# Kernel optimization log

Measured on AMD Instinct MI355X. Metric: run time of the kernel, lower is better.

Reference implementation:

```python
import jax, jax.numpy as jnp
from jax import lax
import numpy as np

T = 8
TAU = 2.0       # LIFNode tau
VTH = 1.0       # v_threshold for IF and LIF
ALPHA = 2.0     # surrogate.ATan default alpha
BN_EPS = 1e-5

# --- ATan surrogate-gradient heaviside (spikingjelly semantics) ---
@jax.custom_vjp
def heaviside_atan(x):
    return (x >= 0.0).astype(x.dtype)

def _h_fwd(x):
    return heaviside_atan(x), x

def _h_bwd(x, g):
    sg = (ALPHA / 2.0) / (1.0 + (jnp.pi / 2.0 * ALPHA * x) ** 2)
    return (g * sg,)

heaviside_atan.defvjp(_h_fwd, _h_bwd)

# --- multi-step IF node: v += x; spike; hard reset to 0 ---
def if_node(x_seq):
    def step(v, x):
        v = v + x
        s = heaviside_atan(v - VTH)
        return (1.0 - s) * v, s
    return lax.scan(step, jnp.zeros_like(x_seq[0]), x_seq)[1]

# --- multi-step LIF node (decay_input=True, v_reset=0, hard reset) ---
def lif_node(x_seq):
    def step(v, x):
        v = v + (x - v) / TAU
        s = heaviside_atan(v - VTH)
        return (1.0 - s) * v, s
    return lax.scan(step, jnp.zeros_like(x_seq[0]), x_seq)[1]

def conv2d(x, w, b):
    y = lax.conv_general_dilated(x, w, (1, 1), 'SAME', dimension_numbers=('NCHW', 'OIHW', 'NCHW'))
    return y + b[None, :, None, None]

def bn(x, g, b, m, v):
    scale = g * lax.rsqrt(v + BN_EPS)
    return (x - m[None, :, None, None]) * scale[None, :, None, None] + b[None, :, None, None]

def maxpool2(x):
    return lax.reduce_window(x, -jnp.inf, lax.max, (1, 1, 2, 2), (1, 1, 2, 2), 'VALID')


def setup_inputs():
    key = jax.random.key(0)
    ks = jax.random.split(key, 8)
    B = 32
    f32 = jnp.float32
    d = {}
    d['x'] = jax.random.normal(ks[0], (B, 1, 48, 48), f32)
    d['conv1_w'] = jax.random.normal(ks[1], (128, 1, 3, 3), f32) * 0.2
    d['conv1_b'] = jnp.zeros((128,), f32)
    d['bn1_g'] = jnp.ones((128,), f32)
    d['bn1_b'] = jnp.zeros((128,), f32)
    d['bn1_m'] = jnp.zeros((128,), f32)
    d['bn1_v'] = jnp.ones((128,), f32)
    d['conv2_w'] = jax.random.normal(ks[2], (128, 128, 3, 3), f32) * 0.03
    d['conv2_b'] = jnp.zeros((128,), f32)
    d['bn2_g'] = jnp.ones((128,), f32)
    d['bn2_b'] = jnp.zeros((128,), f32)
    d['bn2_m'] = jnp.zeros((128,), f32)
    d['bn2_v'] = jnp.ones((128,), f32)
    d['fc1_w'] = jax.random.normal(ks[3], (1152, 128 * 12 * 12), f32) * 0.007
    d['fc1_b'] = jnp.zeros((1152,), f32)
    d['fc2_w'] = jax.random.normal(ks[4], (128, 1152), f32) * 0.03
    d['fc2_b'] = jnp.zeros((128,), f32)
    d['fc3_w'] = jax.random.normal(ks[5], (7, 128), f32) * 0.09
    d['fc3_b'] = jnp.zeros((7,), f32)
    return d


def reference(x, conv1_w, conv1_b, bn1_g, bn1_b, bn1_m, bn1_v,
              conv2_w, conv2_b, bn2_g, bn2_b, bn2_m, bn2_v,
              fc1_w, fc1_b, fc2_w, fc2_b, fc3_w, fc3_b):
    B = x.shape[0]
    # layer1 (single-step): conv + BN (eval-mode), dropout is identity at eval
    h = bn(conv2d(x, conv1_w, conv1_b), bn1_g, bn1_b, bn1_m, bn1_v)  # [B,128,48,48]
    # repeat over T timesteps
    x_step = jnp.broadcast_to(h, (T,) + h.shape)                      # [T,B,128,48,48]
    # layer2: IF -> maxpool -> conv -> BN -> IF -> maxpool
    s1 = if_node(x_step)                                              # [T,B,128,48,48]
    p1 = maxpool2(s1.reshape((T * B,) + s1.shape[2:]))                # [T*B,128,24,24]
    c2 = bn(conv2d(p1, conv2_w, conv2_b), bn2_g, bn2_b, bn2_m, bn2_v)
    s2 = if_node(c2.reshape((T, B) + c2.shape[1:]))                   # [T,B,128,24,24]
    p2 = maxpool2(s2.reshape((T * B,) + s2.shape[2:]))                # [T*B,128,12,12]
    # layer3: flatten -> fc -> LIF -> fc -> LIF -> fc -> LIF
    f = p2.reshape(T, B, -1)                                          # [T,B,18432]
    l1 = lif_node(jnp.einsum('tbi,oi->tbo', f, fc1_w) + fc1_b)        # [T,B,1152]
    l2 = lif_node(jnp.einsum('tbi,oi->tbo', l1, fc2_w) + fc2_b)       # [T,B,128]
    l3 = lif_node(jnp.einsum('tbi,oi->tbo', l2, fc3_w) + fc3_b)       # [T,B,7]
    return l3.mean(axis=0)                                            # [B,7]
```

## Files before the change

### kernel.cpp

```cpp
#include <hip/hip_runtime.h>
#include <hip/hip_bf16.h>


typedef float  f32x4  __attribute__((ext_vector_type(4)));
typedef __bf16 bf16x8 __attribute__((ext_vector_type(8)));

#define T_STEPS 8

static const size_t OFF_P1    = 0;
static const size_t OFF_PART  = 0;
static const size_t OFF_WT    = 44302336;
static const size_t OFF_P2    = 45481984;
static const size_t OFF_W2T   = 54919168;
static const size_t OFF_L1S   = 55508992;

__device__ __forceinline__ unsigned short bf16_rne(float f) {
  unsigned u = __builtin_bit_cast(unsigned, f);
  u += 0x7FFFu + ((u >> 16) & 1u);
  return (unsigned short)(u >> 16);
}
__device__ __forceinline__ float bf16_to_f(unsigned short h) {
  unsigned u = ((unsigned)h) << 16;
  return __builtin_bit_cast(float, u);
}

__device__ __forceinline__ void split_pair(float f0, float f1, unsigned& hi, unsigned& lo) {
  __hip_bfloat162 h2 = __float22bfloat162_rn(make_float2(f0, f1));
  unsigned uh; __builtin_memcpy(&uh, &h2, 4);
  float g0 = __builtin_bit_cast(float, uh << 16);
  float g1 = __builtin_bit_cast(float, uh & 0xFFFF0000u);
  __hip_bfloat162 l2 = __float22bfloat162_rn(make_float2(f0 - g0, f1 - g1));
  unsigned ul; __builtin_memcpy(&ul, &l2, 4);
  hi = uh;
  lo = ul;
}

__device__ __forceinline__ void lds_load16(const void* g, void* l) {
  auto* gp = reinterpret_cast<const __attribute__((address_space(1))) unsigned int*>(
      reinterpret_cast<uintptr_t>(g));
  auto* lp = reinterpret_cast<__attribute__((address_space(3))) unsigned int*>(
      reinterpret_cast<uintptr_t>(l));
  __builtin_amdgcn_global_load_lds(gp, lp, 16, 0, 0);
}

__global__ __launch_bounds__(256) void prep_conv1(
    const float* __restrict__ conv2_w, const float* __restrict__ fc2_w,
    short* __restrict__ wt_hi, short* __restrict__ wt_lo, float* __restrict__ w2t,
    uint4* __restrict__ p1pad4,
    const float* __restrict__ x, const float* __restrict__ w1, const float* __restrict__ b1,
    const float* __restrict__ g1, const float* __restrict__ be1, const float* __restrict__ m1,
    const float* __restrict__ vv1, short* __restrict__ p1) {
  __shared__ float patch[2][16];
  const int bx = blockIdx.x;
  if (bx < 2752) {
    int i = bx * 256 + threadIdx.x;
    if (i < 147456) {
      int tap = i >> 14;
      int oc  = (i >> 7) & 127;
      int ic  = i & 127;
      float wv = conv2_w[oc * 1152 + ic * 9 + tap];
      unsigned short h = bf16_rne(wv);
      wt_hi[i] = (short)h;
      wt_lo[i] = (short)bf16_rne(wv - bf16_to_f(h));
    } else if (i < 294912) {
      int j = i - 147456;
      int o = j & 127, k = j >> 7;
      w2t[j] = fc2_w[o * 1152 + k];
    } else {
      int k = i - 294912;
      int tb = k / 1600;
      int rem = k - tb * 1600;
      int pos = rem >> 4, c8 = rem & 15;
      int y, xx;
      if (pos < 26)      { y = 0;  xx = pos; }
      else if (pos < 52) { y = 25; xx = pos - 26; }
      else { int jj = pos - 52; y = 1 + (jj >> 1); xx = (jj & 1) * 25; }
      p1pad4[(tb * 676 + y * 26 + xx) * 16 + c8] = make_uint4(0u, 0u, 0u, 0u);
    }
    return;
  }
  const int bid  = bx - 2752;
  const int b    = bid / 288;
  const int spp  = bid - b * 288;
  const int half = threadIdx.x >> 7;
  const int sp   = spp * 2 + half;
  const int c    = threadIdx.x & 127;
  const int oy = sp / 24, ox = sp % 24;
  if (c < 16) {
    int py = c >> 2, px = c & 3;
    int iy = 2 * oy - 1 + py, ix = 2 * ox - 1 + px;
    float v = 0.f;
    if (iy >= 0 && iy < 48 && ix >= 0 && ix < 48) v = x[b * 2304 + iy * 48 + ix];
    patch[half][c] = v;
  }
  __syncthreads();
  float w[9];
#pragma unroll
  for (int i = 0; i < 9; ++i) w[i] = w1[c * 9 + i];
  float scale = g1[c] * rsqrtf(vv1[c] + 1e-5f);
  float shift = (b1[c] - m1[c]) * scale + be1[c];
  float h[4];
#pragma unroll
  for (int p = 0; p < 4; ++p) {
    int py = p >> 1, px = p & 1;
    float s = 0.f;
#pragma unroll
    for (int dy = 0; dy < 3; ++dy)
#pragma unroll
      for (int dx = 0; dx < 3; ++dx) s += patch[half][(py + dy) * 4 + (px + dx)] * w[dy * 3 + dx];
    h[p] = s * scale + shift;
  }
  float va = 0.f, vb = 0.f, vc = 0.f, vd = 0.f;
  size_t base = ((size_t)b * 676 + (size_t)(1 + oy) * 26 + (1 + ox)) * 128 + c;
#pragma unroll
  for (int t = 0; t < T_STEPS; ++t) {
    va += h[0]; vb += h[1]; vc += h[2]; vd += h[3];
    bool s0 = va >= 1.f, s1 = vb >= 1.f, s2 = vc >= 1.f, s3 = vd >= 1.f;
    p1[base + (size_t)t * (32 * 676 * 128)] = (s0 | s1 | s2 | s3) ? (short)0x3F80 : (short)0;
    if (s0) va = 0.f; if (s1) vb = 0.f; if (s2) vc = 0.f; if (s3) vd = 0.f;
  }
}

__global__ __launch_bounds__(256, 2) void conv2_gemm(
    const short* __restrict__ p1pad, const short* __restrict__ wt_hi, const short* __restrict__ wt_lo,
    const float* __restrict__ conv2_b, const float* __restrict__ bn2_g, const float* __restrict__ bn2_b,
    const float* __restrict__ bn2_m, const float* __restrict__ bn2_v, short* __restrict__ p2) {
  __shared__ __align__(16) short lds[32768];
  short* ldsA  = lds;
  short* ldsBh = lds + 16384;
  short* ldsBl = lds + 24576;

  const int tid = threadIdx.x;
  const int lane = tid & 63;
  const int w = tid >> 6;
  const int wm = w & 1, wn = w >> 1;
  const int b  = blockIdx.x;
  const int sp = blockIdx.y;
  const int gy = sp / 3;
  const int gx = sp - gy * 3;

  const int g = (lane & 7) ^ (lane >> 3);
  int rowofsA[8], bofs[4];
#pragma unroll
  for (int j = 0; j < 8; ++j) {
    int r = w * 64 + j * 8 + (lane >> 3);
    int t = r >> 5, iy = (r >> 3) & 3, ix = r & 7;
    rowofsA[j] = (((t * 32 + b) * 676) + (4 * gy + iy) * 26 + (8 * gx + ix)) * 128 + g * 8;
  }
#pragma unroll
  for (int j = 0; j < 4; ++j) {
    int n = w * 32 + j * 8 + (lane >> 3);
    bofs[j] = n * 128 + g * 8;
  }

  f32x4 acc[8][4];
#pragma unroll
  for (int mi = 0; mi < 8; ++mi)
#pragma unroll
    for (int ni = 0; ni < 4; ++ni) acc[mi][ni] = (f32x4){0.f, 0.f, 0.f, 0.f};

#pragma unroll 1
  for (int s = 0; s < 18; ++s) {
    const int tap = s >> 1;
    const int kk = (s & 1) << 6;
    const int tapoff = ((tap / 3) * 26 + (tap % 3)) * 128;
    __syncthreads();
#pragma unroll
    for (int j = 0; j < 8; ++j) {
      lds_load16(p1pad + rowofsA[j] + tapoff + kk, ldsA + (w * 64 + j * 8) * 64 + lane * 8);
    }
    const int wtoff = tap * 16384 + kk;
#pragma unroll
    for (int j = 0; j < 4; ++j) {
      lds_load16(wt_hi + wtoff + bofs[j], ldsBh + (w * 32 + j * 8) * 64 + lane * 8);
      lds_load16(wt_lo + wtoff + bofs[j], ldsBl + (w * 32 + j * 8) * 64 + lane * 8);
    }
    __syncthreads();
#pragma unroll
    for (int ks = 0; ks < 2; ++ks) {
      const int cch = ks * 4 + (lane >> 4);
      bf16x8 a[8], bh[4], bl[4];
#pragma unroll
      for (int i = 0; i < 8; ++i) {
        int r = wm * 128 + i * 16 + (lane & 15);
        a[i] = *(const bf16x8*)(ldsA + r * 64 + ((cch ^ (r & 7)) * 8));
      }
#pragma unroll
      for (int i = 0; i < 4; ++i) {
        int n = wn * 64 + i * 16 + (lane & 15);
        bh[i] = *(const bf16x8*)(ldsBh + n * 64 + ((cch ^ (n & 7)) * 8));
        bl[i] = *(const bf16x8*)(ldsBl + n * 64 + ((cch ^ (n & 7)) * 8));
      }
#pragma unroll
      for (int mi = 0; mi < 8; ++mi)
#pragma unroll
        for (int ni = 0; ni < 4; ++ni) {
          acc[mi][ni] = __builtin_amdgcn_mfma_f32_16x16x32_bf16(a[mi], bh[ni], acc[mi][ni], 0, 0, 0);
          acc[mi][ni] = __builtin_amdgcn_mfma_f32_16x16x32_bf16(a[mi], bl[ni], acc[mi][ni], 0, 0, 0);
        }
    }
  }

  float sc[4], sh[4];
#pragma unroll
  for (int ni = 0; ni < 4; ++ni) {
    int oc = wn * 64 + ni * 16 + (lane & 15);
    sc[ni] = bn2_g[oc] * rsqrtf(bn2_v[oc] + 1e-5f);
    sh[ni] = (conv2_b[oc] - bn2_m[oc]) * sc[ni] + bn2_b[oc];
  }
  float* ybuf = (float*)lds;
  const int S = 132;
  float v[32];
#pragma unroll
  for (int q = 0; q < 32; ++q) v[q] = 0.f;
  unsigned short* p2u = (unsigned short*)p2;
  __syncthreads();
#pragma unroll
  for (int q = 0; q < 4; ++q) {
    if (wm == (q >> 1)) {
      const int mib = (q & 1) * 4;
#pragma unroll
      for (int ml = 0; ml < 4; ++ml)
#pragma unroll
        for (int ni = 0; ni < 4; ++ni)
#pragma unroll
          for (int r = 0; r < 4; ++r) {
            int lam = ml * 16 + ((lane >> 4) << 2) + r;
            int col = wn * 64 + ni * 16 + (lane & 15);
            ybuf[lam * S + col] = acc[mib + ml][ni][r] * sc[ni] + sh[ni];
          }
    }
    __syncthreads();
    if (tid < 128) {
      const int oc = tid;
#pragma unroll
      for (int tt = 0; tt < 2; ++tt) {
        int t = 2 * q + tt;
#pragma unroll
        for (int pooly = 0; pooly < 2; ++pooly) {
          unsigned short ov[4];
#pragma unroll
          for (int poolx = 0; poolx < 4; ++poolx) {
            bool any = false;
#pragma unroll
            for (int ry = 0; ry < 2; ++ry)
#pragma unroll
              for (int rx = 0; rx < 2; ++rx) {
                int iy = 2 * pooly + ry, ix = 2 * poolx + rx;
                float xx = ybuf[(tt * 32 + iy * 8 + ix) * S + oc];
                int qi = iy * 8 + ix;
                v[qi] += xx;
                bool ss = v[qi] >= 1.f;
                any |= ss;
                if (ss) v[qi] = 0.f;
              }
            ov[poolx] = any ? (unsigned short)0x3F80 : (unsigned short)0;
          }
          ushort4 o4; o4.x = ov[0]; o4.y = ov[1]; o4.z = ov[2]; o4.w = ov[3];
          *(ushort4*)(p2u + ((size_t)(t * 32 + b) * 128 + oc) * 144 + (2 * gy + pooly) * 12 + 4 * gx) = o4;
        }
      }
    }
    __syncthreads();
  }
}

__global__ __launch_bounds__(512) void fc1_gemm(const short* __restrict__ p2,
                                                const float* __restrict__ fc1_w,
                                                float* __restrict__ part) {
  __shared__ __align__(16) short lds[24576];
  short* ldsA = lds;
  short* ldsBh = lds + 16384;
  short* ldsBl = lds + 20480;

  const int tid = threadIdx.x;
  const int lane = tid & 63;
  const int w = tid >> 6;
  const int wm = w & 3, wn = w >> 2;
  const int nt2 = blockIdx.x;
  const int n0 = nt2 * 64;
  const int kb = blockIdx.y * 576;

  const int g = (lane & 7) ^ (lane >> 3);
  int aofs[4];
#pragma unroll
  for (int j = 0; j < 4; ++j) {
    int r = w * 32 + j * 8 + (lane >> 3);
    aofs[j] = r * 18432 + g * 8;
  }
  const int bn = tid >> 3;
  const int c0 = tid & 7;
  const float* wrow = fc1_w + (size_t)(n0 + bn) * 18432 + c0 * 8;
  const int bpos = (c0 ^ (bn & 7)) * 8;

  f32x4 acc[4][2];
#pragma unroll
  for (int mi = 0; mi < 4; ++mi)
#pragma unroll
    for (int ni = 0; ni < 2; ++ni) acc[mi][ni] = (f32x4){0.f, 0.f, 0.f, 0.f};

  float4 q0, q1;
  {
    const float4* wp = (const float4*)(wrow + kb);
    q0 = wp[0]; q1 = wp[1];
  }

#pragma unroll 1
  for (int s = 0; s < 9; ++s) {
    const int koff = kb + s * 64;
    __syncthreads();
#pragma unroll
    for (int j = 0; j < 4; ++j) {
      lds_load16(p2 + aofs[j] + koff, ldsA + (w * 32 + j * 8) * 64 + lane * 8);
    }
    {
      unsigned h0, h1, h2, h3, l0, l1, l2, l3;
      split_pair(q0.x, q0.y, h0, l0);
      split_pair(q0.z, q0.w, h1, l1);
      split_pair(q1.x, q1.y, h2, l2);
      split_pair(q1.z, q1.w, h3, l3);
      uint4 H; H.x = h0; H.y = h1; H.z = h2; H.w = h3;
      uint4 L; L.x = l0; L.y = l1; L.z = l2; L.w = l3;
      *(uint4*)(ldsBh + bn * 64 + bpos) = H;
      *(uint4*)(ldsBl + bn * 64 + bpos) = L;
    }
    if (s < 8) {
      const float4* wp = (const float4*)(wrow + koff + 64);
      q0 = wp[0]; q1 = wp[1];
    }
    __builtin_amdgcn_sched_barrier(0);
    __syncthreads();
#pragma unroll
    for (int ks = 0; ks < 2; ++ks) {
      bf16x8 a[4], bh[2], bl[2];
      const int cch = ks * 4 + (lane >> 4);
#pragma unroll
      for (int i = 0; i < 4; ++i) {
        int r = wm * 64 + i * 16 + (lane & 15);
        a[i] = *(const bf16x8*)(ldsA + r * 64 + ((cch ^ (r & 7)) * 8));
      }
#pragma unroll
      for (int i = 0; i < 2; ++i) {
        int n = wn * 32 + i * 16 + (lane & 15);
        bh[i] = *(const bf16x8*)(ldsBh + n * 64 + ((cch ^ (n & 7)) * 8));
        bl[i] = *(const bf16x8*)(ldsBl + n * 64 + ((cch ^ (n & 7)) * 8));
      }
#pragma unroll
      for (int mi = 0; mi < 4; ++mi)
#pragma unroll
        for (int ni = 0; ni < 2; ++ni) {
          acc[mi][ni] = __builtin_amdgcn_mfma_f32_16x16x32_bf16(a[mi], bh[ni], acc[mi][ni], 0, 0, 0);
          acc[mi][ni] = __builtin_amdgcn_mfma_f32_16x16x32_bf16(a[mi], bl[ni], acc[mi][ni], 0, 0, 0);
        }
    }
  }
  const int nt = nt2 >> 1;
  const int jbase = (nt2 & 1) * 64;
  const size_t pbase = (size_t)(blockIdx.y * 9 + nt) * 32768;
#pragma unroll
  for (int ni = 0; ni < 2; ++ni) {
    int j = jbase + wn * 32 + ni * 16 + (lane & 15);
#pragma unroll
    for (int mi = 0; mi < 4; ++mi) {
#pragma unroll
      for (int r = 0; r < 4; ++r) {
        int m = wm * 64 + mi * 16 + ((lane >> 4) << 2) + r;
        part[pbase + (size_t)m * 128 + j] = acc[mi][ni][r];
      }
    }
  }
}

__global__ __launch_bounds__(128) void fc1_reduce_lif(const float* __restrict__ part,
                                                      const float* __restrict__ fc1_b,
                                                      float* __restrict__ l1s) {
  int i = blockIdx.x * 128 + threadIdx.x;
  int b = i / 1152, n = i - b * 1152;
  int nt = n >> 7, j = n & 127;
  float bias = fc1_b[n];
  float v = 0.f;
#pragma unroll
  for (int t = 0; t < T_STEPS; ++t) {
    int m = t * 32 + b;
    float vals[32];
#pragma unroll
    for (int ks = 0; ks < 32; ++ks)
      vals[ks] = part[(((size_t)ks * 9 + nt) * 256 + m) * 128 + j];
    float s = bias;
#pragma unroll
    for (int ks = 0; ks < 32; ++ks) s += vals[ks];
    v += (s - v) * 0.5f;
    bool sp = v >= 1.f;
    l1s[(size_t)m * 1152 + n] = sp ? 1.f : 0.f;
    if (sp) v = 0.f;
  }
}

__global__ __launch_bounds__(512) void tail(const float* __restrict__ l1s,
                                            const float* __restrict__ w2t,
                                            const float* __restrict__ b2,
                                            const float* __restrict__ w3,
                                            const float* __restrict__ b3,
                                            float* __restrict__ out) {
  __shared__ float sx[8][1152];
  __shared__ float part2[4][8][128];
  __shared__ float s2[8][128];
  __shared__ float y3[7][8];
  const int b = blockIdx.x;
  const int tid = threadIdx.x;
  for (int i = tid; i < 9216; i += 512) {
    int t = i / 1152, k = i - t * 1152;
    sx[t][k] = l1s[(size_t)(t * 32 + b) * 1152 + k];
  }
  __syncthreads();
  const int o = tid & 127, h = tid >> 7;
  float p[8];
#pragma unroll
  for (int t = 0; t < 8; ++t) p[t] = 0.f;
#pragma unroll 8
  for (int kk = 0; kk < 288; ++kk) {
    int k = h * 288 + kk;
    float wv = w2t[k * 128 + o];
#pragma unroll
    for (int t = 0; t < 8; ++t) p[t] += sx[t][k] * wv;
  }
#pragma unroll
  for (int t = 0; t < 8; ++t) part2[h][t][o] = p[t];
  __syncthreads();
  if (tid < 128) {
    float v = 0.f;
#pragma unroll
    for (int t = 0; t < 8; ++t) {
      float xx = part2[0][t][o] + part2[1][t][o] + part2[2][t][o] + part2[3][t][o] + b2[o];
      v += (xx - v) * 0.5f;
      bool s = v >= 1.f;
      s2[t][o] = s ? 1.f : 0.f;
      if (s) v = 0.f;
    }
  }
  __syncthreads();
  if (tid < 56) {
    int oo = tid >> 3, t = tid & 7;
    float d = 0.f;
    for (int k = 0; k < 128; ++k) d += s2[t][k] * w3[oo * 128 + k];
    y3[oo][t] = d + b3[oo];
  }
  __syncthreads();
  if (tid < 7) {
    float v = 0.f, a = 0.f;
#pragma unroll
    for (int t = 0; t < 8; ++t) {
      float xx = y3[tid][t];
      v += (xx - v) * 0.5f;
      bool s = v >= 1.f;
      a += s ? 1.f : 0.f;
      if (s) v = 0.f;
    }
    out[b * 7 + tid] = a * 0.125f;
  }
}

extern "C" void kernel_launch(void* const* d_in, const int* in_sizes, int n_in,
                              void* d_out, int out_size, void* d_ws, size_t ws_size,
                              hipStream_t stream) {
  const float* x       = (const float*)d_in[0];
  const float* conv1_w = (const float*)d_in[1];
  const float* conv1_b = (const float*)d_in[2];
  const float* bn1_g   = (const float*)d_in[3];
  const float* bn1_b   = (const float*)d_in[4];
  const float* bn1_m   = (const float*)d_in[5];
  const float* bn1_v   = (const float*)d_in[6];
  const float* conv2_w = (const float*)d_in[7];
  const float* conv2_b = (const float*)d_in[8];
  const float* bn2_g   = (const float*)d_in[9];
  const float* bn2_b   = (const float*)d_in[10];
  const float* bn2_m   = (const float*)d_in[11];
  const float* bn2_v   = (const float*)d_in[12];
  const float* fc1_w   = (const float*)d_in[13];
  const float* fc1_b   = (const float*)d_in[14];
  const float* fc2_w   = (const float*)d_in[15];
  const float* fc2_b   = (const float*)d_in[16];
  const float* fc3_w   = (const float*)d_in[17];
  const float* fc3_b   = (const float*)d_in[18];

  char* ws = (char*)d_ws;
  short* p1pad = (short*)(ws + OFF_P1);
  float* part  = (float*)(ws + OFF_PART);
  short* wt_hi = (short*)(ws + OFF_WT);
  short* wt_lo = wt_hi + 147456;
  short* p2    = (short*)(ws + OFF_P2);
  float* w2t   = (float*)(ws + OFF_W2T);
  float* l1s   = (float*)(ws + OFF_L1S);
  float* out   = (float*)d_out;

  prep_conv1<<<11968, 256, 0, stream>>>(conv2_w, fc2_w, wt_hi, wt_lo, w2t, (uint4*)p1pad,
                                        x, conv1_w, conv1_b, bn1_g, bn1_b, bn1_m, bn1_v, p1pad);
  conv2_gemm<<<dim3(32, 18), 256, 0, stream>>>(p1pad, wt_hi, wt_lo, conv2_b, bn2_g, bn2_b, bn2_m, bn2_v, p2);
  fc1_gemm<<<dim3(18, 32), 512, 0, stream>>>(p2, fc1_w, part);
  fc1_reduce_lif<<<288, 128, 0, stream>>>(part, fc1_b, l1s);
  tail<<<32, 512, 0, stream>>>(l1s, w2t, fc2_b, fc3_w, fc3_b, out);
}
```

Measured before the change: 328.1 us.

## Split fc2/fc3 tail into two kernels to spread fc2 across more blocks

The single 32-block tail kernel is split into a fc2 partial-GEMM kernel launched on a 4x32 grid of 1024-thread blocks and a separate fc3/LIF kernel that reduces the partials from global memory. The aim is more parallelism for the fc2 matvec, which previously ran on only 32 blocks. The cost is an extra launch and a round trip of the partials through global memory, reusing the conv2 weight workspace. Each thread now reads its spike row directly from global memory instead of from shared memory.

```diff
diff --git a/kernel.cpp b/kernel.cpp
--- a/kernel.cpp
+++ b/kernel.cpp
@@ -396,42 +396,40 @@
   }
 }
 
-__global__ __launch_bounds__(512) void tail(const float* __restrict__ l1s,
-                                            const float* __restrict__ w2t,
-                                            const float* __restrict__ b2,
-                                            const float* __restrict__ w3,
-                                            const float* __restrict__ b3,
-                                            float* __restrict__ out) {
-  __shared__ float sx[8][1152];
-  __shared__ float part2[4][8][128];
+__global__ __launch_bounds__(1024) void tail_fc2(const float* __restrict__ l1s,
+                                                 const float* __restrict__ w2t,
+                                                 float* __restrict__ part2g) {
+  const int h = blockIdx.x;
+  const int b = blockIdx.y;
+  const int t = threadIdx.x >> 7;
+  const int o = threadIdx.x & 127;
+  const float* sxrow = l1s + (size_t)(t * 32 + b) * 1152;
+  float p = 0.f;
+#pragma unroll 8
+  for (int kk = 0; kk < 288; ++kk) {
+    int k = h * 288 + kk;
+    p += sxrow[k] * w2t[k * 128 + o];
+  }
+  part2g[(((size_t)b * 4 + h) * 8 + t) * 128 + o] = p;
+}
+
+__global__ __launch_bounds__(128) void tail_fc3(const float* __restrict__ part2g,
+                                                const float* __restrict__ b2,
+                                                const float* __restrict__ w3,
+                                                const float* __restrict__ b3,
+                                                float* __restrict__ out) {
   __shared__ float s2[8][128];
   __shared__ float y3[7][8];
   const int b = blockIdx.x;
   const int tid = threadIdx.x;
-  for (int i = tid; i < 9216; i += 512) {
-    int t = i / 1152, k = i - t * 1152;
-    sx[t][k] = l1s[(size_t)(t * 32 + b) * 1152 + k];
-  }
-  __syncthreads();
-  const int o = tid & 127, h = tid >> 7;
-  float p[8];
-#pragma unroll
-  for (int t = 0; t < 8; ++t) p[t] = 0.f;
-#pragma unroll 8
-  for (int kk = 0; kk < 288; ++kk) {
-    int k = h * 288 + kk;
-    float wv = w2t[k * 128 + o];
-#pragma unroll
-    for (int t = 0; t < 8; ++t) p[t] += sx[t][k] * wv;
-  }
-#pragma unroll
-  for (int t = 0; t < 8; ++t) part2[h][t][o] = p[t];
-  __syncthreads();
-  if (tid < 128) {
+  {
+    const int o = tid;
+    const float* pg = part2g + (size_t)b * 4096;
     float v = 0.f;
 #pragma unroll
     for (int t = 0; t < 8; ++t) {
-      float xx = part2[0][t][o] + part2[1][t][o] + part2[2][t][o] + part2[3][t][o] + b2[o];
+      float xx = pg[t * 128 + o] + pg[1024 + t * 128 + o] + pg[2048 + t * 128 + o]
+               + pg[3072 + t * 128 + o] + b2[o];
       v += (xx - v) * 0.5f;
       bool s = v >= 1.f;
       s2[t][o] = s ? 1.f : 0.f;
@@ -488,6 +486,7 @@
   float* part  = (float*)(ws + OFF_PART);
   short* wt_hi = (short*)(ws + OFF_WT);
   short* wt_lo = wt_hi + 147456;
+  float* part2g = (float*)(ws + OFF_WT);
   short* p2    = (short*)(ws + OFF_P2);
   float* w2t   = (float*)(ws + OFF_W2T);
   float* l1s   = (float*)(ws + OFF_L1S);
@@ -498,5 +497,6 @@
   conv2_gemm<<<dim3(32, 18), 256, 0, stream>>>(p1pad, wt_hi, wt_lo, conv2_b, bn2_g, bn2_b, bn2_m, bn2_v, p2);
   fc1_gemm<<<dim3(18, 32), 512, 0, stream>>>(p2, fc1_w, part);
   fc1_reduce_lif<<<288, 128, 0, stream>>>(part, fc1_b, l1s);
-  tail<<<32, 512, 0, stream>>>(l1s, w2t, fc2_b, fc3_w, fc3_b, out);
-}
+  tail_fc2<<<dim3(4, 32), 1024, 0, stream>>>(l1s, w2t, part2g);
+  tail_fc3<<<32, 128, 0, stream>>>(part2g, fc2_b, fc3_w, fc3_b, out);
+}
```

After: 328.5 us. Within noise of the previous version (+0.1%).
